# Performance work log

Hardware: AMD Instinct MI355X
Metric: run time of the kernel (lower is better)

## Reference

```python
import jax, jax.numpy as jnp
import numpy as np

B, T, M, D, H = 32, 256, 16, 128, 128

def _hard_sigmoid(x):
    # Keras hard_sigmoid: clip(0.2*x + 0.5, 0, 1)
    return jnp.clip(0.2 * x + 0.5, 0.0, 1.0)

def setup_inputs() -> dict:
    key = jax.random.key(0)
    ks = jax.random.split(key, 16)
    s = 0.05  # small init scale, roughly glorot-ish for these dims
    inp = {"x": jax.random.normal(ks[0], (B, T, M, D), jnp.float32)}
    inp["W_a"] = jax.random.normal(ks[1], (D + H, H), jnp.float32) * s
    inp["b_a"] = jnp.zeros((H,), jnp.float32)
    for i, n in enumerate("ifco"):
        inp[f"W_{n}"] = jax.random.normal(ks[2 + 3 * i], (D, H), jnp.float32) * s
        inp[f"U_{n}"] = jax.random.normal(ks[3 + 3 * i], (H, H), jnp.float32) * s
        inp[f"b_{n}"] = jnp.ones((H,), jnp.float32) if n == "f" else jnp.zeros((H,), jnp.float32)
    return inp

def reference(x, W_a, b_a, W_i, U_i, b_i, W_f, U_f, b_f, W_c, U_c, b_c, W_o, U_o, b_o):
    b, t, m, d = x.shape
    h_dim = W_i.shape[1]

    def step(carry, x_t):  # x_t: (B, M, D)
        h, c = carry  # each (B, H)
        hb = jnp.broadcast_to(h[:, None, :], (b, m, h_dim))
        con = jnp.concatenate([x_t, hb], axis=-1)          # (B, M, D+H)
        scores = (con @ W_a + b_a).sum(axis=-1)            # (B, M), linear activation
        sm = jax.nn.softmax(scores, axis=-1)               # (B, M)
        new_x = jnp.einsum('bm,bmd->bd', sm, x_t)          # attention-pooled input
        i_g = _hard_sigmoid(new_x @ W_i + b_i + h @ U_i)
        f_g = _hard_sigmoid(new_x @ W_f + b_f + h @ U_f)
        c_new = f_g * c + i_g * jnp.tanh(new_x @ W_c + b_c + h @ U_c)
        o_g = _hard_sigmoid(new_x @ W_o + b_o + h @ U_o)
        h_new = o_g * jnp.tanh(c_new)
        return (h_new, c_new), None

    h0 = jnp.zeros((b, h_dim), x.dtype)
    c0 = jnp.zeros((b, h_dim), x.dtype)
    (h_last, _), _ = jax.lax.scan(step, (h0, c0), jnp.swapaxes(x, 0, 1))
    return h_last  # return_sequences=False -> last output (B, H)
```

## Files before the change

### kernel.cpp

```cpp
#include <hip/hip_runtime.h>
#include <hip/hip_bf16.h>
#include <hip/hip_fp16.h>

#define BB 32
#define TT 256
#define MM 16
#define DD 128
#define HH 128

typedef unsigned int uint;
typedef unsigned short ushort;

typedef _Float16 f16;
typedef _Float16 f16x8 __attribute__((ext_vector_type(8)));
typedef float f32x4 __attribute__((ext_vector_type(4)));

__device__ __forceinline__ float bl16(uint u){ return __uint_as_float(u << 16); }
__device__ __forceinline__ float bh16(uint u){ return __uint_as_float(u & 0xffff0000u); }

__device__ __forceinline__ ushort f2bu(float f){
  __hip_bfloat16 h = __float2bfloat16(f);
  return *(ushort*)&h;
}

__device__ __forceinline__ float hsig(float x){
  return __builtin_amdgcn_fmed3f(fmaf(x, 0.2f, 0.5f), 0.0f, 1.0f);
}
__device__ __forceinline__ float tanh_f(float x){
  return 1.0f - 2.0f / (__expf(2.0f * x) + 1.0f);
}

__device__ __forceinline__ uint packh2(float a, float b){
  __half2 hv = __floats2half2_rn(a, b);
  union{__half2 h; uint x;} cv; cv.h = hv; return cv.x;
}

__global__ __launch_bounds__(128) void k_init(const void* __restrict__ xraw,
                                              const void* __restrict__ Wa,
                                              int* __restrict__ flag,
                                              float* __restrict__ vx){
  __shared__ int cnt[128];
  __shared__ int smode;
  int tid = threadIdx.x;
  const ushort* u = (const ushort*)xraw;
  int c = 0;
  for (int j = 0; j < 16; ++j){
    ushort v = u[2 * (tid * 16 + j)];
    float f = __uint_as_float(((uint)v) << 16);
    if (f == f && fabsf(f) < 64.f && fabsf(f) > 1e-12f) ++c;
  }
  cnt[tid] = c;
  __syncthreads();
  if (tid == 0){
    int s = 0;
    for (int j = 0; j < 128; ++j) s += cnt[j];
    int m = (s > 1024) ? 1 : 0;
    smode = m; *flag = m;
  }
  __syncthreads();
  int mode = smode;

  int d = tid;
  float s = 0.f;
  if (mode){
    const uint4* row = (const uint4*)((const ushort*)Wa + d * HH);
    #pragma unroll
    for (int q = 0; q < 16; ++q){
      uint4 v = row[q];
      s += bl16(v.x) + bh16(v.x) + bl16(v.y) + bh16(v.y)
         + bl16(v.z) + bh16(v.z) + bl16(v.w) + bh16(v.w);
    }
  } else {
    const float4* row = (const float4*)((const float*)Wa + d * HH);
    #pragma unroll
    for (int q = 0; q < 32; ++q){
      float4 v = row[q];
      s += v.x + v.y + v.z + v.w;
    }
  }
  vx[d] = s;
}

__global__ __launch_bounds__(256) void k_uprep2(
  const void* __restrict__ M0, const void* __restrict__ M1,
  const void* __restrict__ M2, const void* __restrict__ M3,
  const int* __restrict__ flag, uint4* __restrict__ dst)
{
  int mode = *flag;
  int idx = blockIdx.x * 256 + threadIdx.x;
  int f = idx >> 6, lane = idx & 63;
  int g = f >> 5, kc = (f >> 3) & 3, w = f & 7;
  int k0 = kc * 32 + (lane >> 4) * 8;
  int c  = w * 16 + (lane & 15);
  const void* Ms[4] = {M0, M1, M2, M3};
  float v[8];
  if (mode){
    const ushort* U = (const ushort*)Ms[g];
    #pragma unroll
    for (int e = 0; e < 8; ++e)
      v[e] = __uint_as_float(((uint)U[(size_t)(k0 + e) * HH + c]) << 16);
  } else {
    const float* U = (const float*)Ms[g];
    #pragma unroll
    for (int e = 0; e < 8; ++e)
      v[e] = U[(size_t)(k0 + e) * HH + c];
  }
  uint4 o;
  o.x = packh2(v[0], v[1]); o.y = packh2(v[2], v[3]);
  o.z = packh2(v[4], v[5]); o.w = packh2(v[6], v[7]);
  dst[idx] = o;
}

__global__ __launch_bounds__(256) void k_pool(const void* __restrict__ xraw,
                                              const int* __restrict__ flag,
                                              const float* __restrict__ vx,
                                              __hip_bfloat16* __restrict__ newx){
  __shared__ float xs[2][MM][DD];
  __shared__ float vxs[DD];
  __shared__ float part[2][128];
  __shared__ float sc[2][MM];
  int mode = *flag;
  int tid = threadIdx.x;
  int half = tid >> 7, t2 = tid & 127;
  int bt = blockIdx.x * 2 + half;
  int b = bt >> 8, t = bt & 255;

  float* xdst = &xs[half][0][0];
  if (mode){
    const uint4* s = (const uint4*)((const ushort*)xraw + (size_t)bt * 2048);
    #pragma unroll
    for (int q = 0; q < 2; ++q){
      int ch = t2 + 128 * q;
      uint4 v = s[ch];
      float* d = &xdst[ch * 8];
      d[0] = bl16(v.x); d[1] = bh16(v.x);
      d[2] = bl16(v.y); d[3] = bh16(v.y);
      d[4] = bl16(v.z); d[5] = bh16(v.z);
      d[6] = bl16(v.w); d[7] = bh16(v.w);
    }
  } else {
    const float4* s = (const float4*)((const float*)xraw + (size_t)bt * 2048);
    #pragma unroll
    for (int q = 0; q < 4; ++q){
      int ch = t2 + 128 * q;
      *(float4*)&xdst[ch * 4] = s[ch];
    }
  }
  if (tid < DD) vxs[tid] = vx[tid];
  __syncthreads();

  int m = t2 >> 3, cc = t2 & 7;
  float p = 0.f;
  #pragma unroll
  for (int j = 0; j < 16; ++j)
    p = fmaf(xs[half][m][cc * 16 + j], vxs[cc * 16 + j], p);
  part[half][t2] = p;
  __syncthreads();
  if (t2 < MM){
    float s = 0.f;
    #pragma unroll
    for (int q = 0; q < 8; ++q) s += part[half][t2 * 8 + q];
    sc[half][t2] = s;
  }
  __syncthreads();

  float mx = sc[half][0];
  #pragma unroll
  for (int m2 = 1; m2 < MM; ++m2) mx = fmaxf(mx, sc[half][m2]);
  float wgt[MM]; float den = 0.f;
  #pragma unroll
  for (int m2 = 0; m2 < MM; ++m2){ wgt[m2] = __expf(sc[half][m2] - mx); den += wgt[m2]; }
  float inv = 1.0f / den;

  float acc = 0.f;
  #pragma unroll
  for (int m2 = 0; m2 < MM; ++m2)
    acc = fmaf(wgt[m2], xs[half][m2][t2], acc);
  newx[((size_t)t * BB + b) * DD + t2] = __float2bfloat16(acc * inv);
}

__global__ __launch_bounds__(256) void k_xproj(const __hip_bfloat16* __restrict__ nx,
  const void* __restrict__ W0, const void* __restrict__ W1,
  const void* __restrict__ W2, const void* __restrict__ W3,
  const void* __restrict__ b0_, const void* __restrict__ b1_,
  const void* __restrict__ b2_, const void* __restrict__ b3_,
  const int* __restrict__ flag, float* __restrict__ Xp)
{
  __shared__ __hip_bfloat16 As[128][DD];
  __shared__ __hip_bfloat16 Ws[DD][HH];
  int mode = *flag;
  int tid = threadIdx.x;
  int r0 = blockIdx.x * 128;
  int g  = blockIdx.y;
  const void* W  = (g == 0) ? W0  : (g == 1) ? W1  : (g == 2) ? W2  : W3;
  const void* bb = (g == 0) ? b0_ : (g == 1) ? b1_ : (g == 2) ? b2_ : b3_;

  const uint4* asrc = (const uint4*)(nx + (size_t)r0 * DD);
  uint4* adst = (uint4*)&As[0][0];
  uint4* wdst = (uint4*)&Ws[0][0];
  #pragma unroll
  for (int q = 0; q < 8; ++q) adst[q * 256 + tid] = asrc[q * 256 + tid];

  if (mode){
    const uint4* wsrc = (const uint4*)W;
    #pragma unroll
    for (int q = 0; q < 8; ++q) wdst[q * 256 + tid] = wsrc[q * 256 + tid];
  } else {
    const float4* wsrc = (const float4*)W;
    #pragma unroll
    for (int q = 0; q < 8; ++q){
      int ch = q * 256 + tid;
      float4 a = wsrc[2 * ch], b = wsrc[2 * ch + 1];
      uint4 o;
      o.x = (uint)f2bu(a.x) | ((uint)f2bu(a.y) << 16);
      o.y = (uint)f2bu(a.z) | ((uint)f2bu(a.w) << 16);
      o.z = (uint)f2bu(b.x) | ((uint)f2bu(b.y) << 16);
      o.w = (uint)f2bu(b.z) | ((uint)f2bu(b.w) << 16);
      wdst[ch] = o;
    }
  }
  __syncthreads();

  int ti = tid >> 4, tj = tid & 15;
  int i0 = ti * 8, j0 = tj * 8;
  float acc[8][8] = {};

  for (int k = 0; k < DD; k += 8){
    float a[8][8];
    #pragma unroll
    for (int ii = 0; ii < 8; ++ii){
      uint4 v = *(const uint4*)&As[i0 + ii][k];
      a[ii][0] = bl16(v.x); a[ii][1] = bh16(v.x);
      a[ii][2] = bl16(v.y); a[ii][3] = bh16(v.y);
      a[ii][4] = bl16(v.z); a[ii][5] = bh16(v.z);
      a[ii][6] = bl16(v.w); a[ii][7] = bh16(v.w);
    }
    #pragma unroll
    for (int kk = 0; kk < 8; ++kk){
      uint4 v = *(const uint4*)&Ws[k + kk][j0];
      float w[8];
      w[0] = bl16(v.x); w[1] = bh16(v.x);
      w[2] = bl16(v.y); w[3] = bh16(v.y);
      w[4] = bl16(v.z); w[5] = bh16(v.z);
      w[6] = bl16(v.w); w[7] = bh16(v.w);
      #pragma unroll
      for (int ii = 0; ii < 8; ++ii)
        #pragma unroll
        for (int jj = 0; jj < 8; ++jj)
          acc[ii][jj] = fmaf(a[ii][kk], w[jj], acc[ii][jj]);
    }
  }

  float bias[8];
  if (mode){
    #pragma unroll
    for (int jj = 0; jj < 8; ++jj)
      bias[jj] = __uint_as_float(((uint)((const ushort*)bb)[j0 + jj]) << 16);
  } else {
    #pragma unroll
    for (int jj = 0; jj < 8; ++jj) bias[jj] = ((const float*)bb)[j0 + jj];
  }
  #pragma unroll
  for (int ii = 0; ii < 8; ++ii){
    size_t r = (size_t)(r0 + i0 + ii);
    float* orow = &Xp[r * 512 + g * HH + j0];
    float4 o1 = make_float4(acc[ii][0] + bias[0], acc[ii][1] + bias[1],
                            acc[ii][2] + bias[2], acc[ii][3] + bias[3]);
    float4 o2 = make_float4(acc[ii][4] + bias[4], acc[ii][5] + bias[5],
                            acc[ii][6] + bias[6], acc[ii][7] + bias[7]);
    *(float4*)orow       = o1;
    *(float4*)(orow + 4) = o2;
  }
}

__global__ __attribute__((amdgpu_waves_per_eu(2, 2))) __launch_bounds__(512)
void k_rec(const float* __restrict__ Xp, const uint4* __restrict__ Uw,
           float* __restrict__ out)
{
  __shared__ __align__(16) __half hlds[2][HH];
  int tid  = threadIdx.x;
  int b    = blockIdx.x;
  int w    = tid >> 6;
  int lane = tid & 63;
  int l16  = lane & 15;

  f16x8 Ub[16];
  #pragma unroll
  for (int g = 0; g < 4; ++g)
    #pragma unroll
    for (int kc = 0; kc < 4; ++kc){
      uint4 v = Uw[((g * 4 + kc) * 8 + w) * 64 + lane];
      union{uint4 u; f16x8 h;} cv; cv.u = v;
      Ub[g * 4 + kc] = cv.h;
    }

  const float* xcol = Xp + (size_t)b * 512 + w * 16 + l16;
  float xpA[4], xpB[4];
  #pragma unroll
  for (int g = 0; g < 4; ++g) xpA[g] = xcol[g * 128];
  #pragma unroll
  for (int g = 0; g < 4; ++g) xpB[g] = xcol[(size_t)(BB * 512) + g * 128];

  if (tid < 64) ((uint*)&hlds[0][0])[tid] = 0;
  float cst = 0.f, vh = 0.f;
  const int lo = (lane >> 4) * 16;
  __syncthreads();

#define STEP(T, XP) do{                                                        \
    const char* hb = (const char*)&hlds[(T) & 1][0];                           \
    f16x8 a0 = *(const f16x8*)(hb +   0 + lo);                                 \
    f16x8 a1 = *(const f16x8*)(hb +  64 + lo);                                 \
    f16x8 a2 = *(const f16x8*)(hb + 128 + lo);                                 \
    f16x8 a3 = *(const f16x8*)(hb + 192 + lo);                                 \
    f32x4 c0 = {XP[0], XP[0], XP[0], XP[0]};                                   \
    f32x4 c1 = {XP[1], XP[1], XP[1], XP[1]};                                   \
    f32x4 c2 = {XP[2], XP[2], XP[2], XP[2]};                                   \
    f32x4 c3 = {XP[3], XP[3], XP[3], XP[3]};                                   \
    c0 = __builtin_amdgcn_mfma_f32_16x16x32_f16(a0, Ub[ 0], c0, 0, 0, 0);      \
    c1 = __builtin_amdgcn_mfma_f32_16x16x32_f16(a0, Ub[ 4], c1, 0, 0, 0);      \
    c2 = __builtin_amdgcn_mfma_f32_16x16x32_f16(a0, Ub[ 8], c2, 0, 0, 0);      \
    c3 = __builtin_amdgcn_mfma_f32_16x16x32_f16(a0, Ub[12], c3, 0, 0, 0);      \
    c0 = __builtin_amdgcn_mfma_f32_16x16x32_f16(a1, Ub[ 1], c0, 0, 0, 0);      \
    c1 = __builtin_amdgcn_mfma_f32_16x16x32_f16(a1, Ub[ 5], c1, 0, 0, 0);      \
    c2 = __builtin_amdgcn_mfma_f32_16x16x32_f16(a1, Ub[ 9], c2, 0, 0, 0);      \
    c3 = __builtin_amdgcn_mfma_f32_16x16x32_f16(a1, Ub[13], c3, 0, 0, 0);      \
    c0 = __builtin_amdgcn_mfma_f32_16x16x32_f16(a2, Ub[ 2], c0, 0, 0, 0);      \
    c1 = __builtin_amdgcn_mfma_f32_16x16x32_f16(a2, Ub[ 6], c1, 0, 0, 0);      \
    c2 = __builtin_amdgcn_mfma_f32_16x16x32_f16(a2, Ub[10], c2, 0, 0, 0);      \
    c3 = __builtin_amdgcn_mfma_f32_16x16x32_f16(a2, Ub[14], c3, 0, 0, 0);      \
    c0 = __builtin_amdgcn_mfma_f32_16x16x32_f16(a3, Ub[ 3], c0, 0, 0, 0);      \
    c1 = __builtin_amdgcn_mfma_f32_16x16x32_f16(a3, Ub[ 7], c1, 0, 0, 0);      \
    c2 = __builtin_amdgcn_mfma_f32_16x16x32_f16(a3, Ub[11], c2, 0, 0, 0);      \
    c3 = __builtin_amdgcn_mfma_f32_16x16x32_f16(a3, Ub[15], c3, 0, 0, 0);      \
    float ig = hsig(c0[0]), fg = hsig(c1[0]), og = hsig(c3[0]);                \
    float gg = tanh_f(c2[0]);                                                  \
    cst = fmaf(fg, cst, ig * gg);                                              \
    vh  = og * tanh_f(cst);                                                    \
    if (lane < 16) hlds[((T) + 1) & 1][w * 16 + lane] = __float2half(vh);      \
    {                                                                          \
      int tp = (T) + 2; if (tp > TT - 1) tp = TT - 1;                          \
      const float* xs = xcol + ((size_t)tp << 14);                             \
      _Pragma("unroll")                                                        \
      for (int g = 0; g < 4; ++g) XP[g] = xs[g * 128];                         \
    }                                                                          \
    asm volatile("s_waitcnt lgkmcnt(0)" ::: "memory");                         \
    __builtin_amdgcn_s_barrier();                                              \
    asm volatile("" ::: "memory");                                             \
  }while(0)

  for (int t = 0; t < TT; t += 2){
    STEP(t,     xpA);
    STEP(t + 1, xpB);
  }
#undef STEP

  if (lane < 16) out[b * HH + w * 16 + lane] = vh;
}

extern "C" void kernel_launch(void* const* d_in, const int* in_sizes, int n_in,
                              void* d_out, int out_size, void* d_ws, size_t ws_size,
                              hipStream_t stream) {
  (void)in_sizes; (void)n_in; (void)out_size; (void)ws_size;

  char* ws = (char*)d_ws;
  int* flag = (int*)ws;
  float* vx = (float*)(ws + 16);
  uint4* Uw = (uint4*)(ws + 1024);
  __hip_bfloat16* newx = (__hip_bfloat16*)(ws + 1024 + 131072);
  float* Xp = (float*)(ws + 1024 + 131072 + (size_t)2 * 1024 * 1024);

  k_init<<<1, 128, 0, stream>>>(d_in[0], d_in[1], flag, vx);
  k_uprep2<<<32, 256, 0, stream>>>(d_in[4], d_in[7], d_in[10], d_in[13], flag, Uw);
  k_pool<<<BB * TT / 2, 256, 0, stream>>>(d_in[0], flag, vx, newx);
  dim3 g2(64, 4);
  k_xproj<<<g2, 256, 0, stream>>>(newx,
      d_in[3], d_in[6], d_in[9], d_in[12],
      d_in[5], d_in[8], d_in[11], d_in[14],
      flag, Xp);
  k_rec<<<BB, 512, 0, stream>>>(Xp, Uw, (float*)d_out);
}
```

Baseline: 269.6 us.

## Merge prep kernels, use MFMA for input projection, split recurrence accumulation chains

The init and U-prep kernels become one k_prep launch, which also packs the W matrices into an fp16 MFMA layout. The input projection changes from scalar bf16 FMAs to fp16 MFMA with a swizzled LDS tile and preloaded bias, and the pooled input is stored as fp16 instead of bf16. In the recurrent step, each gate's four dependent MFMAs become two independent accumulator chains summed at the end, shortening the serial dependency per timestep. The risks are fp16 range and precision differences and the scattered scalar stores of Xp.

```diff
diff --git a/kernel.cpp b/kernel.cpp
--- a/kernel.cpp
+++ b/kernel.cpp
@@ -18,11 +18,6 @@
 __device__ __forceinline__ float bl16(uint u){ return __uint_as_float(u << 16); }
 __device__ __forceinline__ float bh16(uint u){ return __uint_as_float(u & 0xffff0000u); }
 
-__device__ __forceinline__ ushort f2bu(float f){
-  __hip_bfloat16 h = __float2bfloat16(f);
-  return *(ushort*)&h;
-}
-
 __device__ __forceinline__ float hsig(float x){
   return __builtin_amdgcn_fmed3f(fmaf(x, 0.2f, 0.5f), 0.0f, 1.0f);
 }
@@ -35,86 +30,95 @@
   union{__half2 h; uint x;} cv; cv.h = hv; return cv.x;
 }
 
-__global__ __launch_bounds__(128) void k_init(const void* __restrict__ xraw,
-                                              const void* __restrict__ Wa,
-                                              int* __restrict__ flag,
-                                              float* __restrict__ vx){
-  __shared__ int cnt[128];
+__global__ __launch_bounds__(256) void k_prep(
+  const void* __restrict__ xraw, const void* __restrict__ Wa,
+  const void* __restrict__ U0, const void* __restrict__ U1,
+  const void* __restrict__ U2, const void* __restrict__ U3,
+  const void* __restrict__ W0, const void* __restrict__ W1,
+  const void* __restrict__ W2, const void* __restrict__ W3,
+  int* __restrict__ flag, float* __restrict__ vx,
+  uint4* __restrict__ Uw, uint4* __restrict__ Ww)
+{
+  __shared__ int cnt[256];
   __shared__ int smode;
   int tid = threadIdx.x;
-  const ushort* u = (const ushort*)xraw;
-  int c = 0;
-  for (int j = 0; j < 16; ++j){
-    ushort v = u[2 * (tid * 16 + j)];
-    float f = __uint_as_float(((uint)v) << 16);
-    if (f == f && fabsf(f) < 64.f && fabsf(f) > 1e-12f) ++c;
-  }
-  cnt[tid] = c;
-  __syncthreads();
-  if (tid == 0){
-    int s = 0;
-    for (int j = 0; j < 128; ++j) s += cnt[j];
-    int m = (s > 1024) ? 1 : 0;
-    smode = m; *flag = m;
-  }
-  __syncthreads();
+  int bid = blockIdx.x;
+
+  {
+    const ushort* u = (const ushort*)xraw;
+    int c = 0;
+    #pragma unroll
+    for (int j = 0; j < 8; ++j){
+      ushort v = u[2 * (tid * 8 + j)];
+      float f = __uint_as_float(((uint)v) << 16);
+      if (f == f && fabsf(f) < 64.f && fabsf(f) > 1e-12f) ++c;
+    }
+    cnt[tid] = c;
+    __syncthreads();
+    if (tid == 0){
+      int s = 0;
+      for (int i = 0; i < 256; ++i) s += cnt[i];
+      smode = (s > 1024) ? 1 : 0;
+    }
+    __syncthreads();
+  }
   int mode = smode;
 
-  int d = tid;
-  float s = 0.f;
-  if (mode){
-    const uint4* row = (const uint4*)((const ushort*)Wa + d * HH);
-    #pragma unroll
-    for (int q = 0; q < 16; ++q){
-      uint4 v = row[q];
-      s += bl16(v.x) + bh16(v.x) + bl16(v.y) + bh16(v.y)
-         + bl16(v.z) + bh16(v.z) + bl16(v.w) + bh16(v.w);
-    }
+  if (bid < 64){
+    int idx = (bid & 31) * 256 + tid;
+    int f = idx >> 6, lane = idx & 63;
+    int g = f >> 5, kc = (f >> 3) & 3, cb = f & 7;
+    int k0 = kc * 32 + (lane >> 4) * 8;
+    int c  = cb * 16 + (lane & 15);
+    const void* Ms[4];
+    if (bid < 32){ Ms[0] = U0; Ms[1] = U1; Ms[2] = U2; Ms[3] = U3; }
+    else         { Ms[0] = W0; Ms[1] = W1; Ms[2] = W2; Ms[3] = W3; }
+    float v[8];
+    if (mode){
+      const ushort* U = (const ushort*)Ms[g];
+      #pragma unroll
+      for (int e = 0; e < 8; ++e)
+        v[e] = __uint_as_float(((uint)U[(size_t)(k0 + e) * HH + c]) << 16);
+    } else {
+      const float* U = (const float*)Ms[g];
+      #pragma unroll
+      for (int e = 0; e < 8; ++e)
+        v[e] = U[(size_t)(k0 + e) * HH + c];
+    }
+    uint4 o;
+    o.x = packh2(v[0], v[1]); o.y = packh2(v[2], v[3]);
+    o.z = packh2(v[4], v[5]); o.w = packh2(v[6], v[7]);
+    ((bid < 32) ? Uw : Ww)[idx] = o;
   } else {
-    const float4* row = (const float4*)((const float*)Wa + d * HH);
-    #pragma unroll
-    for (int q = 0; q < 32; ++q){
-      float4 v = row[q];
-      s += v.x + v.y + v.z + v.w;
-    }
-  }
-  vx[d] = s;
-}
-
-__global__ __launch_bounds__(256) void k_uprep2(
-  const void* __restrict__ M0, const void* __restrict__ M1,
-  const void* __restrict__ M2, const void* __restrict__ M3,
-  const int* __restrict__ flag, uint4* __restrict__ dst)
-{
-  int mode = *flag;
-  int idx = blockIdx.x * 256 + threadIdx.x;
-  int f = idx >> 6, lane = idx & 63;
-  int g = f >> 5, kc = (f >> 3) & 3, w = f & 7;
-  int k0 = kc * 32 + (lane >> 4) * 8;
-  int c  = w * 16 + (lane & 15);
-  const void* Ms[4] = {M0, M1, M2, M3};
-  float v[8];
-  if (mode){
-    const ushort* U = (const ushort*)Ms[g];
-    #pragma unroll
-    for (int e = 0; e < 8; ++e)
-      v[e] = __uint_as_float(((uint)U[(size_t)(k0 + e) * HH + c]) << 16);
-  } else {
-    const float* U = (const float*)Ms[g];
-    #pragma unroll
-    for (int e = 0; e < 8; ++e)
-      v[e] = U[(size_t)(k0 + e) * HH + c];
-  }
-  uint4 o;
-  o.x = packh2(v[0], v[1]); o.y = packh2(v[2], v[3]);
-  o.z = packh2(v[4], v[5]); o.w = packh2(v[6], v[7]);
-  dst[idx] = o;
+    if (tid == 0) *flag = mode;
+    if (tid < 128){
+      int d = tid;
+      float s = 0.f;
+      if (mode){
+        const uint4* row = (const uint4*)((const ushort*)Wa + d * HH);
+        #pragma unroll
+        for (int q = 0; q < 16; ++q){
+          uint4 v = row[q];
+          s += bl16(v.x) + bh16(v.x) + bl16(v.y) + bh16(v.y)
+             + bl16(v.z) + bh16(v.z) + bl16(v.w) + bh16(v.w);
+        }
+      } else {
+        const float4* row = (const float4*)((const float*)Wa + d * HH);
+        #pragma unroll
+        for (int q = 0; q < 32; ++q){
+          float4 v = row[q];
+          s += v.x + v.y + v.z + v.w;
+        }
+      }
+      vx[d] = s;
+    }
+  }
 }
 
 __global__ __launch_bounds__(256) void k_pool(const void* __restrict__ xraw,
                                               const int* __restrict__ flag,
                                               const float* __restrict__ vx,
-                                              __hip_bfloat16* __restrict__ newx){
+                                              __half* __restrict__ newx){
   __shared__ float xs[2][MM][DD];
   __shared__ float vxs[DD];
   __shared__ float part[2][128];
@@ -176,101 +180,79 @@
   #pragma unroll
   for (int m2 = 0; m2 < MM; ++m2)
     acc = fmaf(wgt[m2], xs[half][m2][t2], acc);
-  newx[((size_t)t * BB + b) * DD + t2] = __float2bfloat16(acc * inv);
-}
-
-__global__ __launch_bounds__(256) void k_xproj(const __hip_bfloat16* __restrict__ nx,
-  const void* __restrict__ W0, const void* __restrict__ W1,
-  const void* __restrict__ W2, const void* __restrict__ W3,
+  newx[((size_t)t * BB + b) * DD + t2] = __float2half(acc * inv);
+}
+
+__global__ __launch_bounds__(256) void k_xproj(const __half* __restrict__ nx,
+  const uint4* __restrict__ Ww,
   const void* __restrict__ b0_, const void* __restrict__ b1_,
   const void* __restrict__ b2_, const void* __restrict__ b3_,
   const int* __restrict__ flag, float* __restrict__ Xp)
 {
-  __shared__ __hip_bfloat16 As[128][DD];
-  __shared__ __hip_bfloat16 Ws[DD][HH];
-  int mode = *flag;
+  __shared__ __align__(16) char As[32768];
   int tid = threadIdx.x;
   int r0 = blockIdx.x * 128;
-  int g  = blockIdx.y;
-  const void* W  = (g == 0) ? W0  : (g == 1) ? W1  : (g == 2) ? W2  : W3;
-  const void* bb = (g == 0) ? b0_ : (g == 1) ? b1_ : (g == 2) ? b2_ : b3_;
-
-  const uint4* asrc = (const uint4*)(nx + (size_t)r0 * DD);
-  uint4* adst = (uint4*)&As[0][0];
-  uint4* wdst = (uint4*)&Ws[0][0];
-  #pragma unroll
-  for (int q = 0; q < 8; ++q) adst[q * 256 + tid] = asrc[q * 256 + tid];
-
-  if (mode){
-    const uint4* wsrc = (const uint4*)W;
-    #pragma unroll
-    for (int q = 0; q < 8; ++q) wdst[q * 256 + tid] = wsrc[q * 256 + tid];
-  } else {
-    const float4* wsrc = (const float4*)W;
-    #pragma unroll
-    for (int q = 0; q < 8; ++q){
-      int ch = q * 256 + tid;
-      float4 a = wsrc[2 * ch], b = wsrc[2 * ch + 1];
-      uint4 o;
-      o.x = (uint)f2bu(a.x) | ((uint)f2bu(a.y) << 16);
-      o.y = (uint)f2bu(a.z) | ((uint)f2bu(a.w) << 16);
-      o.z = (uint)f2bu(b.x) | ((uint)f2bu(b.y) << 16);
-      o.w = (uint)f2bu(b.z) | ((uint)f2bu(b.w) << 16);
-      wdst[ch] = o;
-    }
-  }
-  __syncthreads();
-
-  int ti = tid >> 4, tj = tid & 15;
-  int i0 = ti * 8, j0 = tj * 8;
-  float acc[8][8] = {};
-
-  for (int k = 0; k < DD; k += 8){
-    float a[8][8];
-    #pragma unroll
-    for (int ii = 0; ii < 8; ++ii){
-      uint4 v = *(const uint4*)&As[i0 + ii][k];
-      a[ii][0] = bl16(v.x); a[ii][1] = bh16(v.x);
-      a[ii][2] = bl16(v.y); a[ii][3] = bh16(v.y);
-      a[ii][4] = bl16(v.z); a[ii][5] = bh16(v.z);
-      a[ii][6] = bl16(v.w); a[ii][7] = bh16(v.w);
-    }
-    #pragma unroll
-    for (int kk = 0; kk < 8; ++kk){
-      uint4 v = *(const uint4*)&Ws[k + kk][j0];
-      float w[8];
-      w[0] = bl16(v.x); w[1] = bh16(v.x);
-      w[2] = bl16(v.y); w[3] = bh16(v.y);
-      w[4] = bl16(v.z); w[5] = bh16(v.z);
-      w[6] = bl16(v.w); w[7] = bh16(v.w);
+  int G  = blockIdx.y;
+  int lane = tid & 63, w = tid >> 6;
+  int l16 = lane & 15, lq = lane >> 4;
+
+  {
+    const uint4* src = (const uint4*)(nx + (size_t)r0 * DD);
+    uint4* dst = (uint4*)As;
+    #pragma unroll
+    for (int i = 0; i < 8; ++i){
+      int gid = i * 256 + tid;
+      int r = gid >> 4, c16 = gid & 15;
+      dst[r * 16 + (c16 ^ (r & 15))] = src[gid];
+    }
+  }
+
+  int mode = *flag;
+  const void* bb = (G == 0) ? b0_ : (G == 1) ? b1_ : (G == 2) ? b2_ : b3_;
+  float bias[8];
+  #pragma unroll
+  for (int cb = 0; cb < 8; ++cb){
+    int col = cb * 16 + l16;
+    bias[cb] = mode ? __uint_as_float(((uint)((const ushort*)bb)[col]) << 16)
+                    : ((const float*)bb)[col];
+  }
+  __syncthreads();
+
+  int rb = w * 32;
+  f32x4 acc[2][8];
+  #pragma unroll
+  for (int mt = 0; mt < 2; ++mt)
+    #pragma unroll
+    for (int cb = 0; cb < 8; ++cb)
+      acc[mt][cb] = (f32x4){bias[cb], bias[cb], bias[cb], bias[cb]};
+
+  #pragma unroll
+  for (int kc = 0; kc < 4; ++kc){
+    f16x8 a[2];
+    #pragma unroll
+    for (int mt = 0; mt < 2; ++mt){
+      int r = rb + mt * 16 + l16;
+      int g16 = (kc * 4 + lq) ^ (r & 15);
+      a[mt] = *(const f16x8*)(As + r * 256 + g16 * 16);
+    }
+    #pragma unroll
+    for (int cb = 0; cb < 8; ++cb){
+      union{uint4 u; f16x8 h;} bv;
+      bv.u = Ww[((size_t)((G * 4 + kc) * 8 + cb)) * 64 + lane];
+      acc[0][cb] = __builtin_amdgcn_mfma_f32_16x16x32_f16(a[0], bv.h, acc[0][cb], 0, 0, 0);
+      acc[1][cb] = __builtin_amdgcn_mfma_f32_16x16x32_f16(a[1], bv.h, acc[1][cb], 0, 0, 0);
+    }
+  }
+
+  #pragma unroll
+  for (int mt = 0; mt < 2; ++mt)
+    #pragma unroll
+    for (int cb = 0; cb < 8; ++cb)
       #pragma unroll
-      for (int ii = 0; ii < 8; ++ii)
-        #pragma unroll
-        for (int jj = 0; jj < 8; ++jj)
-          acc[ii][jj] = fmaf(a[ii][kk], w[jj], acc[ii][jj]);
-    }
-  }
-
-  float bias[8];
-  if (mode){
-    #pragma unroll
-    for (int jj = 0; jj < 8; ++jj)
-      bias[jj] = __uint_as_float(((uint)((const ushort*)bb)[j0 + jj]) << 16);
-  } else {
-    #pragma unroll
-    for (int jj = 0; jj < 8; ++jj) bias[jj] = ((const float*)bb)[j0 + jj];
-  }
-  #pragma unroll
-  for (int ii = 0; ii < 8; ++ii){
-    size_t r = (size_t)(r0 + i0 + ii);
-    float* orow = &Xp[r * 512 + g * HH + j0];
-    float4 o1 = make_float4(acc[ii][0] + bias[0], acc[ii][1] + bias[1],
-                            acc[ii][2] + bias[2], acc[ii][3] + bias[3]);
-    float4 o2 = make_float4(acc[ii][4] + bias[4], acc[ii][5] + bias[5],
-                            acc[ii][6] + bias[6], acc[ii][7] + bias[7]);
-    *(float4*)orow       = o1;
-    *(float4*)(orow + 4) = o2;
-  }
+      for (int reg = 0; reg < 4; ++reg){
+        size_t r = (size_t)(r0 + rb + mt * 16 + lq * 4 + reg);
+        Xp[r * 512 + G * HH + cb * 16 + l16] = acc[mt][cb][reg];
+      }
 }
 
 __global__ __attribute__((amdgpu_waves_per_eu(2, 2))) __launch_bounds__(512)
@@ -316,24 +298,32 @@
     f32x4 c1 = {XP[1], XP[1], XP[1], XP[1]};                                   \
     f32x4 c2 = {XP[2], XP[2], XP[2], XP[2]};                                   \
     f32x4 c3 = {XP[3], XP[3], XP[3], XP[3]};                                   \
+    f32x4 d0 = {0.f, 0.f, 0.f, 0.f};                                           \
+    f32x4 d1 = {0.f, 0.f, 0.f, 0.f};                                           \
+    f32x4 d2 = {0.f, 0.f, 0.f, 0.f};                                           \
+    f32x4 d3 = {0.f, 0.f, 0.f, 0.f};                                           \
     c0 = __builtin_amdgcn_mfma_f32_16x16x32_f16(a0, Ub[ 0], c0, 0, 0, 0);      \
     c1 = __builtin_amdgcn_mfma_f32_16x16x32_f16(a0, Ub[ 4], c1, 0, 0, 0);      \
     c2 = __builtin_amdgcn_mfma_f32_16x16x32_f16(a0, Ub[ 8], c2, 0, 0, 0);      \
     c3 = __builtin_amdgcn_mfma_f32_16x16x32_f16(a0, Ub[12], c3, 0, 0, 0);      \
+    d0 = __builtin_amdgcn_mfma_f32_16x16x32_f16(a2, Ub[ 2], d0, 0, 0, 0);      \
+    d1 = __builtin_amdgcn_mfma_f32_16x16x32_f16(a2, Ub[ 6], d1, 0, 0, 0);      \
+    d2 = __builtin_amdgcn_mfma_f32_16x16x32_f16(a2, Ub[10], d2, 0, 0, 0);      \
+    d3 = __builtin_amdgcn_mfma_f32_16x16x32_f16(a2, Ub[14], d3, 0, 0, 0);      \
     c0 = __builtin_amdgcn_mfma_f32_16x16x32_f16(a1, Ub[ 1], c0, 0, 0, 0);      \
     c1 = __builtin_amdgcn_mfma_f32_16x16x32_f16(a1, Ub[ 5], c1, 0, 0, 0);      \
     c2 = __builtin_amdgcn_mfma_f32_16x16x32_f16(a1, Ub[ 9], c2, 0, 0, 0);      \
     c3 = __builtin_amdgcn_mfma_f32_16x16x32_f16(a1, Ub[13], c3, 0, 0, 0);      \
-    c0 = __builtin_amdgcn_mfma_f32_16x16x32_f16(a2, Ub[ 2], c0, 0, 0, 0);      \
-    c1 = __builtin_amdgcn_mfma_f32_16x16x32_f16(a2, Ub[ 6], c1, 0, 0, 0);      \
-    c2 = __builtin_amdgcn_mfma_f32_16x16x32_f16(a2, Ub[10], c2, 0, 0, 0);      \
-    c3 = __builtin_amdgcn_mfma_f32_16x16x32_f16(a2, Ub[14], c3, 0, 0, 0);      \
-    c0 = __builtin_amdgcn_mfma_f32_16x16x32_f16(a3, Ub[ 3], c0, 0, 0, 0);      \
-    c1 = __builtin_amdgcn_mfma_f32_16x16x32_f16(a3, Ub[ 7], c1, 0, 0, 0);      \
-    c2 = __builtin_amdgcn_mfma_f32_16x16x32_f16(a3, Ub[11], c2, 0, 0, 0);      \
-    c3 = __builtin_amdgcn_mfma_f32_16x16x32_f16(a3, Ub[15], c3, 0, 0, 0);      \
-    float ig = hsig(c0[0]), fg = hsig(c1[0]), og = hsig(c3[0]);                \
-    float gg = tanh_f(c2[0]);                                                  \
+    d0 = __builtin_amdgcn_mfma_f32_16x16x32_f16(a3, Ub[ 3], d0, 0, 0, 0);      \
+    d1 = __builtin_amdgcn_mfma_f32_16x16x32_f16(a3, Ub[ 7], d1, 0, 0, 0);      \
+    d2 = __builtin_amdgcn_mfma_f32_16x16x32_f16(a3, Ub[11], d2, 0, 0, 0);      \
+    d3 = __builtin_amdgcn_mfma_f32_16x16x32_f16(a3, Ub[15], d3, 0, 0, 0);      \
+    float p0 = c0[0] + d0[0];                                                  \
+    float p1 = c1[0] + d1[0];                                                  \
+    float p2 = c2[0] + d2[0];                                                  \
+    float p3 = c3[0] + d3[0];                                                  \
+    float ig = hsig(p0), fg = hsig(p1), og = hsig(p3);                         \
+    float gg = tanh_f(p2);                                                     \
     cst = fmaf(fg, cst, ig * gg);                                              \
     vh  = og * tanh_f(cst);                                                    \
     if (lane < 16) hlds[((T) + 1) & 1][w * 16 + lane] = __float2half(vh);      \
@@ -366,15 +356,17 @@
   int* flag = (int*)ws;
   float* vx = (float*)(ws + 16);
   uint4* Uw = (uint4*)(ws + 1024);
-  __hip_bfloat16* newx = (__hip_bfloat16*)(ws + 1024 + 131072);
-  float* Xp = (float*)(ws + 1024 + 131072 + (size_t)2 * 1024 * 1024);
-
-  k_init<<<1, 128, 0, stream>>>(d_in[0], d_in[1], flag, vx);
-  k_uprep2<<<32, 256, 0, stream>>>(d_in[4], d_in[7], d_in[10], d_in[13], flag, Uw);
+  uint4* Ww = (uint4*)(ws + 1024 + 131072);
+  __half* newx = (__half*)(ws + 1024 + 2 * 131072);
+  float* Xp = (float*)(ws + 1024 + 2 * 131072 + (size_t)2 * 1024 * 1024);
+
+  k_prep<<<65, 256, 0, stream>>>(d_in[0], d_in[1],
+      d_in[4], d_in[7], d_in[10], d_in[13],
+      d_in[3], d_in[6], d_in[9],  d_in[12],
+      flag, vx, Uw, Ww);
   k_pool<<<BB * TT / 2, 256, 0, stream>>>(d_in[0], flag, vx, newx);
   dim3 g2(64, 4);
-  k_xproj<<<g2, 256, 0, stream>>>(newx,
-      d_in[3], d_in[6], d_in[9], d_in[12],
+  k_xproj<<<g2, 256, 0, stream>>>(newx, Ww,
       d_in[5], d_in[8], d_in[11], d_in[14],
       flag, Xp);
   k_rec<<<BB, 512, 0, stream>>>(Xp, Uw, (float*)d_out);
```

After: 251.9 us. -6.6%, faster.
